# Kernel optimization log

Hardware: AMD Instinct MI355X
Metric: run time of the kernel (lower is better)

Reference implementation:

```python
import jax, jax.numpy as jnp
import numpy as np

B, N, K = 1, 8192, 32
C_S, C_Z, C_H, H, PQ, PV = 384, 128, 16, 12, 4, 8
CZ4 = C_Z // 4
INF, EPS = 1e5, 1e-8
SOFTPLUS_INV_1 = 0.541324854612918


def _lin(key, i, o):
    return jax.random.normal(key, (i, o), jnp.float32) / np.sqrt(i)


def setup_inputs() -> dict:
    key = jax.random.key(0)
    ks = jax.random.split(key, 20)
    inp = {}
    inp["s"] = jax.random.normal(ks[0], (B, N, C_S), jnp.float32)
    inp["z"] = jax.random.normal(ks[1], (B, N, K, C_Z), jnp.float32)
    inp["edge_index"] = jax.random.randint(ks[2], (B, N, K), 0, N)
    m = jax.random.normal(ks[3], (B, N, 3, 3), jnp.float32)
    q, _ = jnp.linalg.qr(m)  # random orthonormal frames
    inp["rot"] = q
    inp["trans"] = 10.0 * jax.random.normal(ks[4], (B, N, 3), jnp.float32)
    inp["mask"] = jnp.ones((B, N), jnp.float32)
    hc = C_H * H
    inp["w_q"] = _lin(ks[5], C_S, hc); inp["b_q"] = jnp.zeros((hc,), jnp.float32)
    inp["w_kv"] = _lin(ks[6], C_S, 2 * hc); inp["b_kv"] = jnp.zeros((2 * hc,), jnp.float32)
    hpq = H * PQ * 3
    inp["w_qp"] = _lin(ks[7], C_S, hpq); inp["b_qp"] = jnp.zeros((hpq,), jnp.float32)
    hpkv = H * (PQ + PV) * 3
    inp["w_kvp"] = _lin(ks[8], C_S, hpkv); inp["b_kvp"] = jnp.zeros((hpkv,), jnp.float32)
    inp["w_b"] = _lin(ks[9], C_Z, H); inp["b_b"] = jnp.zeros((H,), jnp.float32)
    inp["w_dz"] = _lin(ks[10], C_Z, CZ4); inp["b_dz"] = jnp.zeros((CZ4,), jnp.float32)
    inp["head_weights"] = jnp.full((H,), SOFTPLUS_INV_1, jnp.float32)
    cat_dim = H * (CZ4 + C_H + PV * 4)
    inp["w_out"] = _lin(ks[11], cat_dim, C_S); inp["b_out"] = jnp.zeros((C_S,), jnp.float32)
    return inp


def reference(s, z, edge_index, rot, trans, mask,
              w_q, b_q, w_kv, b_kv, w_qp, b_qp, w_kvp, b_kvp,
              w_b, b_b, w_dz, b_dz, head_weights, w_out, b_out):
    gather = jax.vmap(lambda tab, idx: tab[idx])  # per-batch gather along N

    # scalar q/k/v
    q = (s @ w_q + b_q).reshape(B, N, H, C_H)
    kv = (s @ w_kv + b_kv).reshape(B, N, H, 2 * C_H)
    kv_g = gather(kv, edge_index)                      # [B,N,K,H,2C]
    k_g, v_g = kv_g[..., :C_H], kv_g[..., C_H:]

    # point q/k/v in global frame: layout is 3 stacked chunks (x,y,z)
    def to_pts(x):
        x = x.reshape(B, N, 3, -1).swapaxes(-1, -2)     # [B,N,H*P,3]
        return jnp.einsum('bnij,bnmj->bnmi', rot, x) + trans[:, :, None, :]

    q_pts = to_pts(s @ w_qp + b_qp).reshape(B, N, H, PQ, 3)
    kv_pts = to_pts(s @ w_kvp + b_kvp).reshape(B, N, H, PQ + PV, 3)
    kv_pts_g = gather(kv_pts, edge_index)               # [B,N,K,H,PQ+PV,3]
    k_pts_g, v_pts_g = kv_pts_g[..., :PQ, :], kv_pts_g[..., PQ:, :]

    # attention logits [B,H,N,K]
    a = jnp.einsum('bnhc,bnkhc->bhnk', q, k_g) * np.sqrt(1.0 / (3 * C_H))
    b_pair = z @ w_b + b_b                              # [B,N,K,H]
    a = a + np.sqrt(1.0 / 3) * jnp.transpose(b_pair, (0, 3, 1, 2))

    disp = q_pts[:, :, None] - k_pts_g                  # [B,N,K,H,PQ,3]
    pt_att = jnp.sum(disp * disp, axis=-1)              # [B,N,K,H,PQ]
    hw = jax.nn.softplus(head_weights) * np.sqrt(1.0 / (3 * (PQ * 9.0 / 2)))
    pt_att = -0.5 * jnp.sum(pt_att * hw[None, None, None, :, None], axis=-1)
    a = a + jnp.transpose(pt_att, (0, 3, 1, 2))

    edge_mask = gather(mask, edge_index)                # [B,N,K]
    a = a + (INF * (edge_mask - 1.0))[:, None]
    a = jax.nn.softmax(a, axis=-1)

    # outputs
    o = jnp.einsum('bhnk,bnkhc->bnhc', a, v_g).reshape(B, N, H * C_H)
    o_pt = jnp.einsum('bhnk,bnkhpx->bnhpx', a, v_pts_g)  # global frame
    o_pt = jnp.einsum('bnji,bnhpj->bnhpi', rot, o_pt - trans[:, :, None, None, :])
    o_pt_norm = jnp.sqrt(jnp.sum(o_pt * o_pt, axis=-1) + EPS).reshape(B, N, H * PV)
    o_pt = o_pt.reshape(B, N, H * PV, 3)

    pair_z = z @ w_dz + b_dz                            # [B,N,K,CZ4]
    o_pair = jnp.einsum('bhnk,bnkc->bnhc', a, pair_z).reshape(B, N, H * CZ4)

    cat = jnp.concatenate([o, o_pt[..., 0], o_pt[..., 1], o_pt[..., 2],
                           o_pt_norm, o_pair], axis=-1)
    return cat @ w_out + b_out
```

## Files before the change

kernel.cpp:

```cpp
#include <hip/hip_runtime.h>
#include <hip/hip_bf16.h>
#include <math.h>

#define N_NODES 8192
#define KNN 32

typedef unsigned short ushort_t;
typedef ushort_t ushort8 __attribute__((ext_vector_type(8)));
typedef ushort_t ushort4v __attribute__((ext_vector_type(4)));
typedef short short8v __attribute__((ext_vector_type(8)));
typedef float f32x4 __attribute__((ext_vector_type(4)));

static __device__ __forceinline__ float b2f(ushort_t u) {
    union { float f; unsigned int i; } v; v.i = ((unsigned int)u) << 16; return v.f;
}
static __device__ __forceinline__ ushort_t f2b(float f) {
    __hip_bfloat16 h = __float2bfloat16(f);
    return *(ushort_t*)&h;
}

__global__ __launch_bounds__(256) void gemm_bf16(
    const float* __restrict__ A, const float* __restrict__ W,
    const float* __restrict__ bias, float* __restrict__ C,
    int M, int K, int P)
{
    __shared__ ushort_t As[128][40];
    __shared__ ushort_t Bs[128][40];

    const int tid  = threadIdx.x;
    const int ncol = P >> 7;
    const int id   = blockIdx.x;
    const int xcd  = id & 7;
    const int qq   = id >> 3;
    const int row0 = ((qq / ncol) * 8 + xcd) * 128;
    const int col0 = (qq % ncol) * 128;

    const int wave = tid >> 6;
    const int lane = tid & 63;
    const int wm = (wave >> 1) * 64;
    const int wn = (wave & 1) * 64;
    const int m16 = lane & 15;
    const int kof = (lane >> 4) * 8;

    const int a_row = tid >> 1;
    const int a_kq  = (tid & 1) * 16;
    const int b_n  = tid >> 1;
    const int b_kq = (tid & 1) * 16;

    f32x4 acc[4][4];
#pragma unroll
    for (int i = 0; i < 4; ++i)
#pragma unroll
        for (int j = 0; j < 4; ++j) acc[i][j] = (f32x4)0.0f;

    for (int k0 = 0; k0 < K; k0 += 32) {
        {
            const float* ap = A + (size_t)(row0 + a_row) * K + (k0 + a_kq);
            float4 v0 = *(const float4*)(ap);
            float4 v1 = *(const float4*)(ap + 4);
            float4 v2 = *(const float4*)(ap + 8);
            float4 v3 = *(const float4*)(ap + 12);
            ushort8 u0, u1;
            u0[0] = f2b(v0.x); u0[1] = f2b(v0.y); u0[2] = f2b(v0.z); u0[3] = f2b(v0.w);
            u0[4] = f2b(v1.x); u0[5] = f2b(v1.y); u0[6] = f2b(v1.z); u0[7] = f2b(v1.w);
            u1[0] = f2b(v2.x); u1[1] = f2b(v2.y); u1[2] = f2b(v2.z); u1[3] = f2b(v2.w);
            u1[4] = f2b(v3.x); u1[5] = f2b(v3.y); u1[6] = f2b(v3.z); u1[7] = f2b(v3.w);
            *(ushort8*)&As[a_row][a_kq]     = u0;
            *(ushort8*)&As[a_row][a_kq + 8] = u1;
        }
        {
            const int col = col0 + b_n;
            const float* wp = W + (size_t)(k0 + b_kq) * P + col;
            ushort8 u0, u1;
#pragma unroll
            for (int i = 0; i < 8; ++i) { u0[i] = f2b(*wp); wp += P; }
#pragma unroll
            for (int i = 0; i < 8; ++i) { u1[i] = f2b(*wp); wp += P; }
            *(ushort8*)&Bs[b_n][b_kq]     = u0;
            *(ushort8*)&Bs[b_n][b_kq + 8] = u1;
        }
        __syncthreads();

        short8v a[4], b[4];
#pragma unroll
        for (int mb = 0; mb < 4; ++mb)
            a[mb] = *(const short8v*)&As[wm + mb * 16 + m16][kof];
#pragma unroll
        for (int nb = 0; nb < 4; ++nb)
            b[nb] = *(const short8v*)&Bs[wn + nb * 16 + m16][kof];
#pragma unroll
        for (int mb = 0; mb < 4; ++mb)
#pragma unroll
            for (int nb = 0; nb < 4; ++nb)
                acc[mb][nb] = __builtin_amdgcn_mfma_f32_16x16x32_bf16(
                    a[mb], b[nb], acc[mb][nb], 0, 0, 0);
        __syncthreads();
    }

    const int r_base = row0 + wm + (lane >> 4) * 4;
#pragma unroll
    for (int nb = 0; nb < 4; ++nb) {
        const int col = col0 + wn + nb * 16 + m16;
        const float bv = bias[col];
#pragma unroll
        for (int mb = 0; mb < 4; ++mb) {
#pragma unroll
            for (int r = 0; r < 4; ++r) {
                C[(size_t)(r_base + mb * 16 + r) * P + col] = acc[mb][nb][r] + bv;
            }
        }
    }
}

__global__ __launch_bounds__(256) void gemm_out(
    const ushort_t* __restrict__ A, const float* __restrict__ W,
    const float* __restrict__ bias, float* __restrict__ C,
    int M, int K, int P)
{
    __shared__ ushort_t As[64][40];
    __shared__ ushort_t Bs[64][40];

    const int tid  = threadIdx.x;
    const int ncol = P >> 6;
    const int id   = blockIdx.x;
    const int xcd  = id & 7;
    const int qq   = id >> 3;
    const int row0 = ((qq / ncol) * 8 + xcd) * 64;
    const int col0 = (qq % ncol) * 64;

    const int wave = tid >> 6;
    const int lane = tid & 63;
    const int wm = (wave >> 1) * 32;
    const int wn = (wave & 1) * 32;
    const int m16 = lane & 15;
    const int kof = (lane >> 4) * 8;

    const int a_row = tid >> 2;
    const int a_kq  = (tid & 3) * 8;

    f32x4 acc[2][2];
#pragma unroll
    for (int i = 0; i < 2; ++i)
#pragma unroll
        for (int j = 0; j < 2; ++j) acc[i][j] = (f32x4)0.0f;

    for (int k0 = 0; k0 < K; k0 += 32) {
        *(ushort8*)&As[a_row][a_kq] =
            *(const ushort8*)(A + (size_t)(row0 + a_row) * K + (k0 + a_kq));
        {
            const int col = col0 + a_row;
            const float* wp = W + (size_t)(k0 + a_kq) * P + col;
            ushort8 u;
#pragma unroll
            for (int i = 0; i < 8; ++i) { u[i] = f2b(*wp); wp += P; }
            *(ushort8*)&Bs[a_row][a_kq] = u;
        }
        __syncthreads();

        short8v a[2], b[2];
#pragma unroll
        for (int mb = 0; mb < 2; ++mb)
            a[mb] = *(const short8v*)&As[wm + mb * 16 + m16][kof];
#pragma unroll
        for (int nb = 0; nb < 2; ++nb)
            b[nb] = *(const short8v*)&Bs[wn + nb * 16 + m16][kof];
#pragma unroll
        for (int mb = 0; mb < 2; ++mb)
#pragma unroll
            for (int nb = 0; nb < 2; ++nb)
                acc[mb][nb] = __builtin_amdgcn_mfma_f32_16x16x32_bf16(
                    a[mb], b[nb], acc[mb][nb], 0, 0, 0);
        __syncthreads();
    }

    const int r_base = row0 + wm + (lane >> 4) * 4;
#pragma unroll
    for (int nb = 0; nb < 2; ++nb) {
        const int col = col0 + wn + nb * 16 + m16;
        const float bv = bias[col];
#pragma unroll
        for (int mb = 0; mb < 2; ++mb) {
#pragma unroll
            for (int r = 0; r < 4; ++r) {
                C[(size_t)(r_base + mb * 16 + r) * P + col] = acc[mb][nb][r] + bv;
            }
        }
    }
}

__global__ __launch_bounds__(256) void gemm_zproj(
    const float* __restrict__ Z, const float* __restrict__ Wc,
    const float* __restrict__ bc, ushort_t* __restrict__ zph)
{
    __shared__ ushort_t As[64][40];
    __shared__ ushort_t Bs[64][40];

    const int tid  = threadIdx.x;
    const int row0 = blockIdx.x * 64;

    const int wave = tid >> 6;
    const int lane = tid & 63;
    const int wm = (wave >> 1) * 32;
    const int wn = (wave & 1) * 32;
    const int m16 = lane & 15;
    const int kof = (lane >> 4) * 8;

    const int a_row = tid >> 2;
    const int a_kq  = (tid & 3) * 8;

    f32x4 acc[2][2];
#pragma unroll
    for (int i = 0; i < 2; ++i)
#pragma unroll
        for (int j = 0; j < 2; ++j) acc[i][j] = (f32x4)0.0f;

    for (int k0 = 0; k0 < 128; k0 += 32) {
        {
            const float* ap = Z + (size_t)(row0 + a_row) * 128 + (k0 + a_kq);
            float4 v0 = *(const float4*)(ap);
            float4 v1 = *(const float4*)(ap + 4);
            ushort8 u;
            u[0] = f2b(v0.x); u[1] = f2b(v0.y); u[2] = f2b(v0.z); u[3] = f2b(v0.w);
            u[4] = f2b(v1.x); u[5] = f2b(v1.y); u[6] = f2b(v1.z); u[7] = f2b(v1.w);
            *(ushort8*)&As[a_row][a_kq] = u;
        }
        {
            const int col = a_row;
            ushort8 u;
            if (col < 44) {
                const float* wp = Wc + (size_t)(k0 + a_kq) * 44 + col;
#pragma unroll
                for (int i = 0; i < 8; ++i) { u[i] = f2b(*wp); wp += 44; }
            } else {
                u = (ushort8)0;
            }
            *(ushort8*)&Bs[a_row][a_kq] = u;
        }
        __syncthreads();

        short8v a[2], b[2];
#pragma unroll
        for (int mb = 0; mb < 2; ++mb)
            a[mb] = *(const short8v*)&As[wm + mb * 16 + m16][kof];
#pragma unroll
        for (int nb = 0; nb < 2; ++nb)
            b[nb] = *(const short8v*)&Bs[wn + nb * 16 + m16][kof];
#pragma unroll
        for (int mb = 0; mb < 2; ++mb)
#pragma unroll
            for (int nb = 0; nb < 2; ++nb)
                acc[mb][nb] = __builtin_amdgcn_mfma_f32_16x16x32_bf16(
                    a[mb], b[nb], acc[mb][nb], 0, 0, 0);
        __syncthreads();
    }

    const int r_base = row0 + wm + (lane >> 4) * 4;
#pragma unroll
    for (int nb = 0; nb < 2; ++nb) {
        const int col = wn + nb * 16 + m16;
        if (col >= 44) continue;
        const float bv = bc[col];
#pragma unroll
        for (int mb = 0; mb < 2; ++mb) {
#pragma unroll
            for (int r = 0; r < 4; ++r) {
                zph[(size_t)(r_base + mb * 16 + r) * 48 + col] = f2b(acc[mb][nb][r] + bv);
            }
        }
    }
}

__global__ void build_wall(const float* __restrict__ wq,  const float* __restrict__ bq,
                           const float* __restrict__ wkv, const float* __restrict__ bkv,
                           const float* __restrict__ wqp, const float* __restrict__ bqp,
                           const float* __restrict__ wkvp,const float* __restrict__ bkvp,
                           float* __restrict__ Wall, float* __restrict__ ball)
{
    int t = blockIdx.x * 256 + threadIdx.x;
    if (t < 384 * 1152) {
        int c = t / 1152, j = t % 1152;
        float v;
        if      (j < 192)  v = wq  [c * 192 + j];
        else if (j < 576)  v = wkv [c * 384 + (j - 192)];
        else if (j < 720)  v = wqp [c * 144 + (j - 576)];
        else               v = wkvp[c * 432 + (j - 720)];
        Wall[t] = v;
    }
    if (t < 1152) {
        float v;
        if      (t < 192)  v = bq[t];
        else if (t < 576)  v = bkv[t - 192];
        else if (t < 720)  v = bqp[t - 576];
        else               v = bkvp[t - 720];
        ball[t] = v;
    }
}

__global__ void build_wcat(const float* __restrict__ wb, const float* __restrict__ bb,
                           const float* __restrict__ wdz, const float* __restrict__ bdz,
                           float* __restrict__ Wcat, float* __restrict__ bcat)
{
    int t = blockIdx.x * 256 + threadIdx.x;
    if (t < 128 * 44) {
        int c = t / 44, j = t % 44;
        Wcat[t] = (j < 12) ? wb[c * 12 + j] : wdz[c * 32 + (j - 12)];
    }
    if (t < 44) bcat[t] = (t < 12) ? bb[t] : bdz[t - 12];
}

__global__ void prep_tables(const float* __restrict__ proj_all,
                            const float* __restrict__ rot,
                            const float* __restrict__ trans,
                            float* __restrict__ q_pts,
                            float* __restrict__ kpt,
                            ushort_t* __restrict__ vpt,
                            ushort_t* __restrict__ kbt,
                            ushort_t* __restrict__ vbt)
{
    int t = blockIdx.x * 256 + threadIdx.x;
    if (t >= N_NODES * 576) return;
    const int n = t / 576;
    const int m = t % 576;
    const float* row = proj_all + (size_t)n * 1152;

    if (m >= 192) {
        const int c0 = m - 192;
        const int h = c0 >> 5, c = c0 & 31;
        ushort_t v = f2b(row[192 + c0]);
        if (c < 16) kbt[(size_t)n * 192 + h * 16 + c] = v;
        else        vbt[(size_t)n * 192 + h * 16 + (c - 16)] = v;
        return;
    }

    const float* R  = rot + n * 9;
    const float* tr = trans + n * 3;
    float X, Y, Z;
    if (m < 48) {
        const float* src = row + 576;
        X = src[m]; Y = src[48 + m]; Z = src[96 + m];
        float gx = R[0] * X + R[1] * Y + R[2] * Z + tr[0];
        float gy = R[3] * X + R[4] * Y + R[5] * Z + tr[1];
        float gz = R[6] * X + R[7] * Y + R[8] * Z + tr[2];
        const int h = m >> 2, p = m & 3;
        float* dst = q_pts + (size_t)n * 144 + h * 12 + p * 3;
        dst[0] = gx; dst[1] = gy; dst[2] = gz;
    } else {
        const int pt = m - 48;
        const int h = pt / 12, p = pt % 12;
        const float* src = row + 720;
        X = src[pt]; Y = src[144 + pt]; Z = src[288 + pt];
        float gx = R[0] * X + R[1] * Y + R[2] * Z + tr[0];
        float gy = R[3] * X + R[4] * Y + R[5] * Z + tr[1];
        float gz = R[6] * X + R[7] * Y + R[8] * Z + tr[2];
        if (p < 4) {
            float* dst = kpt + (size_t)n * 144 + h * 12 + p * 3;
            dst[0] = gx; dst[1] = gy; dst[2] = gz;
        } else {
            ushort_t* dst = vpt + (size_t)n * 288 + h * 24 + (p - 4) * 3;
            dst[0] = f2b(gx); dst[1] = f2b(gy); dst[2] = f2b(gz);
        }
    }
}

__global__ __launch_bounds__(256, 8) void attn_kernel(
    const float* __restrict__ q,
    const ushort_t* __restrict__ kbt,
    const ushort_t* __restrict__ vbt,
    const float* __restrict__ q_pts,
    const float* __restrict__ kpt,
    const ushort_t* __restrict__ vpt,
    const ushort_t* __restrict__ zph,
    const int*   __restrict__ eidx,
    const float* __restrict__ mask,
    const float* __restrict__ rot,
    const float* __restrict__ trans,
    const float* __restrict__ head_weights,
    ushort_t* __restrict__ catb)
{
    const int n   = blockIdx.x;
    const int tid = threadIdx.x;

    __shared__ ushort_t zp[32][48];
    __shared__ float q_s[192];
    __shared__ float qp_s[144];
    __shared__ float a_s[12][33];
    __shared__ float opt[288];
    __shared__ int   idx_s[32];
    __shared__ float madd_s[32];
    __shared__ float R_s[9];
    __shared__ float t_s[3];
    __shared__ float hw_s[12];

    for (int i = tid; i < 192; i += 256) q_s[i]  = q[(size_t)n * 1152 + i];
    for (int i = tid; i < 144; i += 256) qp_s[i] = q_pts[(size_t)n * 144 + i];
    if (tid < 32) {
        const int ix = eidx[n * 32 + tid];
        idx_s[tid]  = ix;
        madd_s[tid] = 100000.0f * (mask[ix] - 1.0f);
    }
    if (tid >= 32 && tid < 41) R_s[tid - 32]  = rot[n * 9 + (tid - 32)];
    if (tid >= 41 && tid < 44) t_s[tid - 41]  = trans[n * 3 + (tid - 41)];
    if (tid >= 44 && tid < 56) {
        float x = head_weights[tid - 44];
        hw_s[tid - 44] = log1pf(__expf(x)) * 0.13608276348795434f;
    }
    if (tid < 192) {
        const int r = tid / 6, sg = tid % 6;
        *(ushort8*)&zp[r][sg * 8] =
            *(const ushort8*)(zph + ((size_t)n * 32 + r) * 48 + sg * 8);
    }
    __syncthreads();

    for (int t = tid; t < 384; t += 256) {
        const int h = t >> 5, j = t & 31;
        const int ix = idx_s[j];
        const ushort_t* kr = kbt + (size_t)ix * 192 + h * 16;
        ushort8 k0 = *(const ushort8*)(kr);
        ushort8 k1 = *(const ushort8*)(kr + 8);
        const float* kpr = kpt + (size_t)ix * 144 + h * 12;
        float4 p0 = *(const float4*)(kpr);
        float4 p1 = *(const float4*)(kpr + 4);
        float4 p2 = *(const float4*)(kpr + 8);

        const float* qh = q_s + h * 16;
        float dot = 0.0f;
#pragma unroll
        for (int c = 0; c < 8; ++c) dot += qh[c] * b2f(k0[c]);
#pragma unroll
        for (int c = 0; c < 8; ++c) dot += qh[8 + c] * b2f(k1[c]);

        const float* qp = qp_s + h * 12;
        float d, pt = 0.0f;
        d = qp[0]  - p0.x; pt += d * d;  d = qp[1]  - p0.y; pt += d * d;
        d = qp[2]  - p0.z; pt += d * d;  d = qp[3]  - p0.w; pt += d * d;
        d = qp[4]  - p1.x; pt += d * d;  d = qp[5]  - p1.y; pt += d * d;
        d = qp[6]  - p1.z; pt += d * d;  d = qp[7]  - p1.w; pt += d * d;
        d = qp[8]  - p2.x; pt += d * d;  d = qp[9]  - p2.y; pt += d * d;
        d = qp[10] - p2.z; pt += d * d;  d = qp[11] - p2.w; pt += d * d;

        a_s[h][j] = 0.14433756729740643f * dot
                  + 0.5773502691896258f * b2f(zp[j][h])
                  - 0.5f * hw_s[h] * pt
                  + madd_s[j];
    }
    __syncthreads();

    if (tid < 96) {
        const int h = tid >> 3, g = tid & 7;
        float a0 = a_s[h][g * 4 + 0], a1 = a_s[h][g * 4 + 1];
        float a2 = a_s[h][g * 4 + 2], a3 = a_s[h][g * 4 + 3];
        float m = fmaxf(fmaxf(a0, a1), fmaxf(a2, a3));
        m = fmaxf(m, __shfl_xor(m, 1)); m = fmaxf(m, __shfl_xor(m, 2));
        m = fmaxf(m, __shfl_xor(m, 4));
        float e0 = __expf(a0 - m), e1 = __expf(a1 - m);
        float e2 = __expf(a2 - m), e3 = __expf(a3 - m);
        float s = e0 + e1 + e2 + e3;
        s += __shfl_xor(s, 1); s += __shfl_xor(s, 2); s += __shfl_xor(s, 4);
        const float inv = 1.0f / s;
        a_s[h][g * 4 + 0] = e0 * inv; a_s[h][g * 4 + 1] = e1 * inv;
        a_s[h][g * 4 + 2] = e2 * inv; a_s[h][g * 4 + 3] = e3 * inv;
    }
    __syncthreads();

    ushort_t* catn = catb + (size_t)n * 960;
    if (tid < 48) {
        const int h = tid >> 2, cq = tid & 3;
        const ushort_t* base = vbt + h * 16 + cq * 4;
        float s0 = 0, s1 = 0, s2 = 0, s3 = 0;
#pragma unroll 8
        for (int j = 0; j < 32; ++j) {
            const int ix = idx_s[j];
            const float aj = a_s[h][j];
            ushort4v v = *(const ushort4v*)(base + (size_t)ix * 192);
            s0 += aj * b2f(v[0]); s1 += aj * b2f(v[1]);
            s2 += aj * b2f(v[2]); s3 += aj * b2f(v[3]);
        }
        ushort4v o = { f2b(s0), f2b(s1), f2b(s2), f2b(s3) };
        *(ushort4v*)&catn[h * 16 + cq * 4] = o;
    } else if (tid < 120) {
        const int u = tid - 48;
        const int h = u / 6, rq = u % 6;
        const ushort_t* base = vpt + h * 24 + rq * 4;
        float s0 = 0, s1 = 0, s2 = 0, s3 = 0;
#pragma unroll 8
        for (int j = 0; j < 32; ++j) {
            const int ix = idx_s[j];
            const float aj = a_s[h][j];
            ushort4v v = *(const ushort4v*)(base + (size_t)ix * 288);
            s0 += aj * b2f(v[0]); s1 += aj * b2f(v[1]);
            s2 += aj * b2f(v[2]); s3 += aj * b2f(v[3]);
        }
        float* od = opt + h * 24 + rq * 4;
        od[0] = s0; od[1] = s1; od[2] = s2; od[3] = s3;
    } else if (tid < 216) {
        const int u = tid - 120;
        const int h = u >> 3, cq = u & 7;
        float s0 = 0, s1 = 0, s2 = 0, s3 = 0;
#pragma unroll 8
        for (int j = 0; j < 32; ++j) {
            const float aj = a_s[h][j];
            ushort4v zv = *(const ushort4v*)&zp[j][12 + cq * 4];
            s0 += aj * b2f(zv[0]); s1 += aj * b2f(zv[1]);
            s2 += aj * b2f(zv[2]); s3 += aj * b2f(zv[3]);
        }
        ushort4v o = { f2b(s0), f2b(s1), f2b(s2), f2b(s3) };
        *(ushort4v*)&catn[576 + h * 32 + cq * 4] = o;
    }
    __syncthreads();

    if (tid < 96) {
        const int h = tid >> 3, p = tid & 7;
        const float* ob = opt + h * 24 + p * 3;
        float gx = ob[0] - t_s[0];
        float gy = ob[1] - t_s[1];
        float gz = ob[2] - t_s[2];
        float lx = R_s[0] * gx + R_s[3] * gy + R_s[6] * gz;
        float ly = R_s[1] * gx + R_s[4] * gy + R_s[7] * gz;
        float lz = R_s[2] * gx + R_s[5] * gy + R_s[8] * gz;
        const int hp = h * 8 + p;
        catn[192 + hp] = f2b(lx);
        catn[288 + hp] = f2b(ly);
        catn[384 + hp] = f2b(lz);
        catn[480 + hp] = f2b(sqrtf(lx * lx + ly * ly + lz * lz + 1e-8f));
    }
}

extern "C" void kernel_launch(void* const* d_in, const int* in_sizes, int n_in,
                              void* d_out, int out_size, void* d_ws, size_t ws_size,
                              hipStream_t stream)
{
    const float* s     = (const float*)d_in[0];
    const float* z     = (const float*)d_in[1];
    const int*   eidx  = (const int*)  d_in[2];
    const float* rot   = (const float*)d_in[3];
    const float* trans = (const float*)d_in[4];
    const float* mask  = (const float*)d_in[5];
    const float* w_q   = (const float*)d_in[6];
    const float* b_q   = (const float*)d_in[7];
    const float* w_kv  = (const float*)d_in[8];
    const float* b_kv  = (const float*)d_in[9];
    const float* w_qp  = (const float*)d_in[10];
    const float* b_qp  = (const float*)d_in[11];
    const float* w_kvp = (const float*)d_in[12];
    const float* b_kvp = (const float*)d_in[13];
    const float* w_b   = (const float*)d_in[14];
    const float* b_b   = (const float*)d_in[15];
    const float* w_dz  = (const float*)d_in[16];
    const float* b_dz  = (const float*)d_in[17];
    const float* hw    = (const float*)d_in[18];
    const float* w_out = (const float*)d_in[19];
    const float* b_out = (const float*)d_in[20];
    float* out = (float*)d_out;

    float* ws = (float*)d_ws;
    size_t off = 0;
    float* proj_all = ws + off; off += (size_t)N_NODES * 1152;
    float* q_pts    = ws + off; off += (size_t)N_NODES * 144;
    float* kpt      = ws + off; off += (size_t)N_NODES * 144;
    ushort_t* vpt   = (ushort_t*)(ws + off); off += (size_t)N_NODES * 144;
    ushort_t* kbt   = (ushort_t*)(ws + off); off += (size_t)N_NODES * 96;
    ushort_t* vbt   = (ushort_t*)(ws + off); off += (size_t)N_NODES * 96;
    ushort_t* zph   = (ushort_t*)(ws + off); off += (size_t)N_NODES * KNN * 24;
    ushort_t* catb  = (ushort_t*)(ws + off); off += (size_t)N_NODES * 480;
    float* Wall     = ws + off; off += (size_t)384 * 1152;
    float* ball     = ws + off; off += 1152;
    float* Wcat     = ws + off; off += 128 * 44;
    float* bcat     = ws + off; off += 44;

    build_wall<<<(384 * 1152 + 255) / 256, 256, 0, stream>>>(
        w_q, b_q, w_kv, b_kv, w_qp, b_qp, w_kvp, b_kvp, Wall, ball);
    gemm_bf16<<<(N_NODES / 128) * 9, 256, 0, stream>>>(s, Wall, ball, proj_all,
                                                       N_NODES, 384, 1152);

    build_wcat<<<23, 256, 0, stream>>>(w_b, b_b, w_dz, b_dz, Wcat, bcat);
    gemm_zproj<<<(N_NODES * KNN) / 64, 256, 0, stream>>>(z, Wcat, bcat, zph);

    prep_tables<<<(N_NODES * 576 + 255) / 256, 256, 0, stream>>>(
        proj_all, rot, trans, q_pts, kpt, vpt, kbt, vbt);

    attn_kernel<<<N_NODES, 256, 0, stream>>>(
        proj_all, kbt, vbt, q_pts, kpt, vpt, zph, eidx, mask, rot, trans, hw, catb);

    gemm_out<<<(N_NODES / 64) * 6, 256, 0, stream>>>(catb, w_out, b_out, out,
                                                     N_NODES, 960, 384);
}
```

Baseline: 188.1 us.

## Pretranspose weights to bf16 once and fuse projection epilogue into table writes

One build_weights kernel now transposes and converts all weight matrices (Wall, Wcat, Wout) to bf16 in N-major layout, so the GEMM B-tile loads become contiguous 16-byte vector loads instead of strided scalar fp32 loads with per-element conversion. The s-projection GEMM epilogue writes q, k and v directly as bf16 into their per-head tables and writes only the point columns in fp32. The prep kernel then handles only the point transforms, which cuts the intermediate fp32 traffic. In exchange q now passes through bf16 before attention, a small precision loss, and the weight preparation adds a full transpose of w_out on every call.

New measurement: 158.4 us. 15.8% less time.

```diff
diff --git a/kernel.cpp b/kernel.cpp
--- a/kernel.cpp
+++ b/kernel.cpp
@@ -19,21 +19,73 @@
     return *(ushort_t*)&h;
 }
 
-__global__ __launch_bounds__(256) void gemm_bf16(
-    const float* __restrict__ A, const float* __restrict__ W,
-    const float* __restrict__ bias, float* __restrict__ C,
-    int M, int K, int P)
+#define N_WALLT (1152 * 384)
+#define N_WCATT (64 * 128)
+#define N_WOUTT (384 * 960)
+__global__ void build_weights(
+    const float* __restrict__ wq,  const float* __restrict__ bq,
+    const float* __restrict__ wkv, const float* __restrict__ bkv,
+    const float* __restrict__ wqp, const float* __restrict__ bqp,
+    const float* __restrict__ wkvp,const float* __restrict__ bkvp,
+    const float* __restrict__ wb,  const float* __restrict__ bb,
+    const float* __restrict__ wdz, const float* __restrict__ bdz,
+    const float* __restrict__ wout,
+    ushort_t* __restrict__ WallT, float* __restrict__ ball,
+    ushort_t* __restrict__ WcatT, float* __restrict__ bcat,
+    ushort_t* __restrict__ WoutT)
+{
+    int t = blockIdx.x * 256 + threadIdx.x;
+    if (t < N_WALLT) {
+        const int p = t / 384, k = t % 384;
+        float v;
+        if      (p < 192) v = wq  [k * 192 + p];
+        else if (p < 576) v = wkv [k * 384 + (p - 192)];
+        else if (p < 720) v = wqp [k * 144 + (p - 576)];
+        else              v = wkvp[k * 432 + (p - 720)];
+        WallT[t] = f2b(v);
+    } else if (t < N_WALLT + N_WCATT) {
+        const int u = t - N_WALLT;
+        const int j = u >> 7, c = u & 127;
+        float v = (j < 12) ? wb[c * 12 + j] : (j < 44 ? wdz[c * 32 + (j - 12)] : 0.0f);
+        WcatT[u] = f2b(v);
+    } else if (t < N_WALLT + N_WCATT + N_WOUTT) {
+        const int u = t - N_WALLT - N_WCATT;
+        const int p = u / 960, k = u % 960;
+        WoutT[u] = f2b(wout[k * 384 + p]);
+    } else {
+        const int u = t - N_WALLT - N_WCATT - N_WOUTT;
+        if (u < 1152) {
+            float v;
+            if      (u < 192)  v = bq[u];
+            else if (u < 576)  v = bkv[u - 192];
+            else if (u < 720)  v = bqp[u - 576];
+            else               v = bkvp[u - 720];
+            ball[u] = v;
+        } else if (u < 1152 + 44) {
+            const int w = u - 1152;
+            bcat[w] = (w < 12) ? bb[w] : bdz[w - 12];
+        }
+    }
+}
+#define BW_TOTAL (N_WALLT + N_WCATT + N_WOUTT + 1152 + 44)
+
+__global__ __launch_bounds__(256) void gemm_sproj(
+    const float* __restrict__ A, const ushort_t* __restrict__ WT,
+    const float* __restrict__ bias,
+    ushort_t* __restrict__ qb, ushort_t* __restrict__ kbt,
+    ushort_t* __restrict__ vbt, float* __restrict__ praw)
 {
     __shared__ ushort_t As[128][40];
     __shared__ ushort_t Bs[128][40];
 
     const int tid  = threadIdx.x;
-    const int ncol = P >> 7;
+    const int ncol = 9;
     const int id   = blockIdx.x;
     const int xcd  = id & 7;
     const int qq   = id >> 3;
     const int row0 = ((qq / ncol) * 8 + xcd) * 128;
     const int col0 = (qq % ncol) * 128;
+    const int K    = 384;
 
     const int wave = tid >> 6;
     const int lane = tid & 63;
@@ -44,8 +96,6 @@
 
     const int a_row = tid >> 1;
     const int a_kq  = (tid & 1) * 16;
-    const int b_n  = tid >> 1;
-    const int b_kq = (tid & 1) * 16;
 
     f32x4 acc[4][4];
 #pragma unroll
@@ -69,15 +119,9 @@
             *(ushort8*)&As[a_row][a_kq + 8] = u1;
         }
         {
-            const int col = col0 + b_n;
-            const float* wp = W + (size_t)(k0 + b_kq) * P + col;
-            ushort8 u0, u1;
-#pragma unroll
-            for (int i = 0; i < 8; ++i) { u0[i] = f2b(*wp); wp += P; }
-#pragma unroll
-            for (int i = 0; i < 8; ++i) { u1[i] = f2b(*wp); wp += P; }
-            *(ushort8*)&Bs[b_n][b_kq]     = u0;
-            *(ushort8*)&Bs[b_n][b_kq + 8] = u1;
+            const ushort_t* wp = WT + (size_t)(col0 + a_row) * K + (k0 + a_kq);
+            *(ushort8*)&Bs[a_row][a_kq]     = *(const ushort8*)(wp);
+            *(ushort8*)&Bs[a_row][a_kq + 8] = *(const ushort8*)(wp + 8);
         }
         __syncthreads();
 
@@ -106,90 +150,24 @@
         for (int mb = 0; mb < 4; ++mb) {
 #pragma unroll
             for (int r = 0; r < 4; ++r) {
-                C[(size_t)(r_base + mb * 16 + r) * P + col] = acc[mb][nb][r] + bv;
+                const int row = r_base + mb * 16 + r;
+                const float v = acc[mb][nb][r] + bv;
+                if (col < 192) {
+                    qb[(size_t)row * 192 + col] = f2b(v);
+                } else if (col < 576) {
+                    const int u = col - 192, h = u >> 5, c = u & 31;
+                    if (c < 16) kbt[(size_t)row * 192 + h * 16 + c] = f2b(v);
+                    else        vbt[(size_t)row * 192 + h * 16 + (c - 16)] = f2b(v);
+                } else {
+                    praw[(size_t)row * 576 + (col - 576)] = v;
+                }
             }
         }
     }
 }
 
-__global__ __launch_bounds__(256) void gemm_out(
-    const ushort_t* __restrict__ A, const float* __restrict__ W,
-    const float* __restrict__ bias, float* __restrict__ C,
-    int M, int K, int P)
-{
-    __shared__ ushort_t As[64][40];
-    __shared__ ushort_t Bs[64][40];
-
-    const int tid  = threadIdx.x;
-    const int ncol = P >> 6;
-    const int id   = blockIdx.x;
-    const int xcd  = id & 7;
-    const int qq   = id >> 3;
-    const int row0 = ((qq / ncol) * 8 + xcd) * 64;
-    const int col0 = (qq % ncol) * 64;
-
-    const int wave = tid >> 6;
-    const int lane = tid & 63;
-    const int wm = (wave >> 1) * 32;
-    const int wn = (wave & 1) * 32;
-    const int m16 = lane & 15;
-    const int kof = (lane >> 4) * 8;
-
-    const int a_row = tid >> 2;
-    const int a_kq  = (tid & 3) * 8;
-
-    f32x4 acc[2][2];
-#pragma unroll
-    for (int i = 0; i < 2; ++i)
-#pragma unroll
-        for (int j = 0; j < 2; ++j) acc[i][j] = (f32x4)0.0f;
-
-    for (int k0 = 0; k0 < K; k0 += 32) {
-        *(ushort8*)&As[a_row][a_kq] =
-            *(const ushort8*)(A + (size_t)(row0 + a_row) * K + (k0 + a_kq));
-        {
-            const int col = col0 + a_row;
-            const float* wp = W + (size_t)(k0 + a_kq) * P + col;
-            ushort8 u;
-#pragma unroll
-            for (int i = 0; i < 8; ++i) { u[i] = f2b(*wp); wp += P; }
-            *(ushort8*)&Bs[a_row][a_kq] = u;
-        }
-        __syncthreads();
-
-        short8v a[2], b[2];
-#pragma unroll
-        for (int mb = 0; mb < 2; ++mb)
-            a[mb] = *(const short8v*)&As[wm + mb * 16 + m16][kof];
-#pragma unroll
-        for (int nb = 0; nb < 2; ++nb)
-            b[nb] = *(const short8v*)&Bs[wn + nb * 16 + m16][kof];
-#pragma unroll
-        for (int mb = 0; mb < 2; ++mb)
-#pragma unroll
-            for (int nb = 0; nb < 2; ++nb)
-                acc[mb][nb] = __builtin_amdgcn_mfma_f32_16x16x32_bf16(
-                    a[mb], b[nb], acc[mb][nb], 0, 0, 0);
-        __syncthreads();
-    }
-
-    const int r_base = row0 + wm + (lane >> 4) * 4;
-#pragma unroll
-    for (int nb = 0; nb < 2; ++nb) {
-        const int col = col0 + wn + nb * 16 + m16;
-        const float bv = bias[col];
-#pragma unroll
-        for (int mb = 0; mb < 2; ++mb) {
-#pragma unroll
-            for (int r = 0; r < 4; ++r) {
-                C[(size_t)(r_base + mb * 16 + r) * P + col] = acc[mb][nb][r] + bv;
-            }
-        }
-    }
-}
-
 __global__ __launch_bounds__(256) void gemm_zproj(
-    const float* __restrict__ Z, const float* __restrict__ Wc,
+    const float* __restrict__ Z, const ushort_t* __restrict__ WcT,
     const float* __restrict__ bc, ushort_t* __restrict__ zph)
 {
     __shared__ ushort_t As[64][40];
@@ -224,18 +202,8 @@
             u[4] = f2b(v1.x); u[5] = f2b(v1.y); u[6] = f2b(v1.z); u[7] = f2b(v1.w);
             *(ushort8*)&As[a_row][a_kq] = u;
         }
-        {
-            const int col = a_row;
-            ushort8 u;
-            if (col < 44) {
-                const float* wp = Wc + (size_t)(k0 + a_kq) * 44 + col;
-#pragma unroll
-                for (int i = 0; i < 8; ++i) { u[i] = f2b(*wp); wp += 44; }
-            } else {
-                u = (ushort8)0;
-            }
-            *(ushort8*)&Bs[a_row][a_kq] = u;
-        }
+        *(ushort8*)&Bs[a_row][a_kq] =
+            *(const ushort8*)(WcT + (size_t)a_row * 128 + (k0 + a_kq));
         __syncthreads();
 
         short8v a[2], b[2];
@@ -270,88 +238,103 @@
     }
 }
 
-__global__ void build_wall(const float* __restrict__ wq,  const float* __restrict__ bq,
-                           const float* __restrict__ wkv, const float* __restrict__ bkv,
-                           const float* __restrict__ wqp, const float* __restrict__ bqp,
-                           const float* __restrict__ wkvp,const float* __restrict__ bkvp,
-                           float* __restrict__ Wall, float* __restrict__ ball)
+__global__ __launch_bounds__(256) void gemm_out(
+    const ushort_t* __restrict__ A, const ushort_t* __restrict__ WT,
+    const float* __restrict__ bias, float* __restrict__ C)
+{
+    __shared__ ushort_t As[64][40];
+    __shared__ ushort_t Bs[64][40];
+
+    const int tid  = threadIdx.x;
+    const int ncol = 6;
+    const int id   = blockIdx.x;
+    const int xcd  = id & 7;
+    const int qq   = id >> 3;
+    const int row0 = ((qq / ncol) * 8 + xcd) * 64;
+    const int col0 = (qq % ncol) * 64;
+    const int K = 960, P = 384;
+
+    const int wave = tid >> 6;
+    const int lane = tid & 63;
+    const int wm = (wave >> 1) * 32;
+    const int wn = (wave & 1) * 32;
+    const int m16 = lane & 15;
+    const int kof = (lane >> 4) * 8;
+
+    const int a_row = tid >> 2;
+    const int a_kq  = (tid & 3) * 8;
+
+    f32x4 acc[2][2];
+#pragma unroll
+    for (int i = 0; i < 2; ++i)
+#pragma unroll
+        for (int j = 0; j < 2; ++j) acc[i][j] = (f32x4)0.0f;
+
+    for (int k0 = 0; k0 < K; k0 += 32) {
+        *(ushort8*)&As[a_row][a_kq] =
+            *(const ushort8*)(A + (size_t)(row0 + a_row) * K + (k0 + a_kq));
+        *(ushort8*)&Bs[a_row][a_kq] =
+            *(const ushort8*)(WT + (size_t)(col0 + a_row) * K + (k0 + a_kq));
+        __syncthreads();
+
+        short8v a[2], b[2];
+#pragma unroll
+        for (int mb = 0; mb < 2; ++mb)
+            a[mb] = *(const short8v*)&As[wm + mb * 16 + m16][kof];
+#pragma unroll
+        for (int nb = 0; nb < 2; ++nb)
+            b[nb] = *(const short8v*)&Bs[wn + nb * 16 + m16][kof];
+#pragma unroll
+        for (int mb = 0; mb < 2; ++mb)
+#pragma unroll
+            for (int nb = 0; nb < 2; ++nb)
+                acc[mb][nb] = __builtin_amdgcn_mfma_f32_16x16x32_bf16(
+                    a[mb], b[nb], acc[mb][nb], 0, 0, 0);
+        __syncthreads();
+    }
+
+    const int r_base = row0 + wm + (lane >> 4) * 4;
+#pragma unroll
+    for (int nb = 0; nb < 2; ++nb) {
+        const int col = col0 + wn + nb * 16 + m16;
+        const float bv = bias[col];
+#pragma unroll
+        for (int mb = 0; mb < 2; ++mb) {
+#pragma unroll
+            for (int r = 0; r < 4; ++r) {
+                C[(size_t)(r_base + mb * 16 + r) * P + col] = acc[mb][nb][r] + bv;
+            }
+        }
+    }
+}
+
+__global__ void prep_pts(const float* __restrict__ praw,
+                         const float* __restrict__ rot,
+                         const float* __restrict__ trans,
+                         float* __restrict__ q_pts,
+                         float* __restrict__ kpt,
+                         ushort_t* __restrict__ vpt)
 {
     int t = blockIdx.x * 256 + threadIdx.x;
-    if (t < 384 * 1152) {
-        int c = t / 1152, j = t % 1152;
-        float v;
-        if      (j < 192)  v = wq  [c * 192 + j];
-        else if (j < 576)  v = wkv [c * 384 + (j - 192)];
-        else if (j < 720)  v = wqp [c * 144 + (j - 576)];
-        else               v = wkvp[c * 432 + (j - 720)];
-        Wall[t] = v;
-    }
-    if (t < 1152) {
-        float v;
-        if      (t < 192)  v = bq[t];
-        else if (t < 576)  v = bkv[t - 192];
-        else if (t < 720)  v = bqp[t - 576];
-        else               v = bkvp[t - 720];
-        ball[t] = v;
-    }
-}
-
-__global__ void build_wcat(const float* __restrict__ wb, const float* __restrict__ bb,
-                           const float* __restrict__ wdz, const float* __restrict__ bdz,
-                           float* __restrict__ Wcat, float* __restrict__ bcat)
-{
-    int t = blockIdx.x * 256 + threadIdx.x;
-    if (t < 128 * 44) {
-        int c = t / 44, j = t % 44;
-        Wcat[t] = (j < 12) ? wb[c * 12 + j] : wdz[c * 32 + (j - 12)];
-    }
-    if (t < 44) bcat[t] = (t < 12) ? bb[t] : bdz[t - 12];
-}
-
-__global__ void prep_tables(const float* __restrict__ proj_all,
-                            const float* __restrict__ rot,
-                            const float* __restrict__ trans,
-                            float* __restrict__ q_pts,
-                            float* __restrict__ kpt,
-                            ushort_t* __restrict__ vpt,
-                            ushort_t* __restrict__ kbt,
-                            ushort_t* __restrict__ vbt)
-{
-    int t = blockIdx.x * 256 + threadIdx.x;
-    if (t >= N_NODES * 576) return;
-    const int n = t / 576;
-    const int m = t % 576;
-    const float* row = proj_all + (size_t)n * 1152;
-
-    if (m >= 192) {
-        const int c0 = m - 192;
-        const int h = c0 >> 5, c = c0 & 31;
-        ushort_t v = f2b(row[192 + c0]);
-        if (c < 16) kbt[(size_t)n * 192 + h * 16 + c] = v;
-        else        vbt[(size_t)n * 192 + h * 16 + (c - 16)] = v;
-        return;
-    }
-
+    if (t >= N_NODES * 192) return;
+    const int n = t / 192;
+    const int m = t % 192;
+    const float* row = praw + (size_t)n * 576;
     const float* R  = rot + n * 9;
     const float* tr = trans + n * 3;
     float X, Y, Z;
+    if (m < 48) { X = row[m];       Y = row[48 + m];   Z = row[96 + m]; }
+    else { const int pt = m - 48;
+           X = row[144 + pt];  Y = row[288 + pt]; Z = row[432 + pt]; }
+    const float gx = R[0] * X + R[1] * Y + R[2] * Z + tr[0];
+    const float gy = R[3] * X + R[4] * Y + R[5] * Z + tr[1];
+    const float gz = R[6] * X + R[7] * Y + R[8] * Z + tr[2];
     if (m < 48) {
-        const float* src = row + 576;
-        X = src[m]; Y = src[48 + m]; Z = src[96 + m];
-        float gx = R[0] * X + R[1] * Y + R[2] * Z + tr[0];
-        float gy = R[3] * X + R[4] * Y + R[5] * Z + tr[1];
-        float gz = R[6] * X + R[7] * Y + R[8] * Z + tr[2];
         const int h = m >> 2, p = m & 3;
         float* dst = q_pts + (size_t)n * 144 + h * 12 + p * 3;
         dst[0] = gx; dst[1] = gy; dst[2] = gz;
     } else {
-        const int pt = m - 48;
-        const int h = pt / 12, p = pt % 12;
-        const float* src = row + 720;
-        X = src[pt]; Y = src[144 + pt]; Z = src[288 + pt];
-        float gx = R[0] * X + R[1] * Y + R[2] * Z + tr[0];
-        float gy = R[3] * X + R[4] * Y + R[5] * Z + tr[1];
-        float gz = R[6] * X + R[7] * Y + R[8] * Z + tr[2];
+        const int pt = m - 48, h = pt / 12, p = pt % 12;
         if (p < 4) {
             float* dst = kpt + (size_t)n * 144 + h * 12 + p * 3;
             dst[0] = gx; dst[1] = gy; dst[2] = gz;
@@ -363,7 +346,7 @@
 }
 
 __global__ __launch_bounds__(256, 8) void attn_kernel(
-    const float* __restrict__ q,
+    const ushort_t* __restrict__ qb,
     const ushort_t* __restrict__ kbt,
     const ushort_t* __restrict__ vbt,
     const float* __restrict__ q_pts,
@@ -391,7 +374,7 @@
     __shared__ float t_s[3];
     __shared__ float hw_s[12];
 
-    for (int i = tid; i < 192; i += 256) q_s[i]  = q[(size_t)n * 1152 + i];
+    for (int i = tid; i < 192; i += 256) q_s[i]  = b2f(qb[(size_t)n * 192 + i]);
     for (int i = tid; i < 144; i += 256) qp_s[i] = q_pts[(size_t)n * 144 + i];
     if (tid < 32) {
         const int ix = eidx[n * 32 + tid];
@@ -554,33 +537,35 @@
 
     float* ws = (float*)d_ws;
     size_t off = 0;
-    float* proj_all = ws + off; off += (size_t)N_NODES * 1152;
-    float* q_pts    = ws + off; off += (size_t)N_NODES * 144;
-    float* kpt      = ws + off; off += (size_t)N_NODES * 144;
-    ushort_t* vpt   = (ushort_t*)(ws + off); off += (size_t)N_NODES * 144;
+    ushort_t* qb    = (ushort_t*)(ws + off); off += (size_t)N_NODES * 96;
     ushort_t* kbt   = (ushort_t*)(ws + off); off += (size_t)N_NODES * 96;
     ushort_t* vbt   = (ushort_t*)(ws + off); off += (size_t)N_NODES * 96;
+    float* praw     = ws + off;              off += (size_t)N_NODES * 576;
+    float* q_pts    = ws + off;              off += (size_t)N_NODES * 144;
+    float* kpt      = ws + off;              off += (size_t)N_NODES * 144;
+    ushort_t* vpt   = (ushort_t*)(ws + off); off += (size_t)N_NODES * 144;
     ushort_t* zph   = (ushort_t*)(ws + off); off += (size_t)N_NODES * KNN * 24;
     ushort_t* catb  = (ushort_t*)(ws + off); off += (size_t)N_NODES * 480;
-    float* Wall     = ws + off; off += (size_t)384 * 1152;
-    float* ball     = ws + off; off += 1152;
-    float* Wcat     = ws + off; off += 128 * 44;
-    float* bcat     = ws + off; off += 44;
-
-    build_wall<<<(384 * 1152 + 255) / 256, 256, 0, stream>>>(
-        w_q, b_q, w_kv, b_kv, w_qp, b_qp, w_kvp, b_kvp, Wall, ball);
-    gemm_bf16<<<(N_NODES / 128) * 9, 256, 0, stream>>>(s, Wall, ball, proj_all,
-                                                       N_NODES, 384, 1152);
-
-    build_wcat<<<23, 256, 0, stream>>>(w_b, b_b, w_dz, b_dz, Wcat, bcat);
-    gemm_zproj<<<(N_NODES * KNN) / 64, 256, 0, stream>>>(z, Wcat, bcat, zph);
-
-    prep_tables<<<(N_NODES * 576 + 255) / 256, 256, 0, stream>>>(
-        proj_all, rot, trans, q_pts, kpt, vpt, kbt, vbt);
+    ushort_t* WallT = (ushort_t*)(ws + off); off += N_WALLT / 2;
+    float* ball     = ws + off;              off += 1152;
+    ushort_t* WcatT = (ushort_t*)(ws + off); off += N_WCATT / 2;
+    float* bcat     = ws + off;              off += 44;
+    ushort_t* WoutT = (ushort_t*)(ws + off); off += N_WOUTT / 2;
+
+    build_weights<<<(BW_TOTAL + 255) / 256, 256, 0, stream>>>(
+        w_q, b_q, w_kv, b_kv, w_qp, b_qp, w_kvp, b_kvp,
+        w_b, b_b, w_dz, b_dz, w_out, WallT, ball, WcatT, bcat, WoutT);
+
+    gemm_sproj<<<(N_NODES / 128) * 9, 256, 0, stream>>>(
+        s, WallT, ball, qb, kbt, vbt, praw);
+
+    gemm_zproj<<<(N_NODES * KNN) / 64, 256, 0, stream>>>(z, WcatT, bcat, zph);
+
+    prep_pts<<<(N_NODES * 192 + 255) / 256, 256, 0, stream>>>(
+        praw, rot, trans, q_pts, kpt, vpt);
 
     attn_kernel<<<N_NODES, 256, 0, stream>>>(
-        proj_all, kbt, vbt, q_pts, kpt, vpt, zph, eidx, mask, rot, trans, hw, catb);
-
-    gemm_out<<<(N_NODES / 64) * 6, 256, 0, stream>>>(catb, w_out, b_out, out,
-                                                     N_NODES, 960, 384);
-}
+        qb, kbt, vbt, q_pts, kpt, vpt, zph, eidx, mask, rot, trans, hw, catb);
+
+    gemm_out<<<(N_NODES / 64) * 6, 256, 0, stream>>>(catb, WoutT, b_out, out);
+}
```
